# Kernel tuning notes

Measured on AMD Instinct MI355X. Metric: run time of the kernel, lower is better.

Reference implementation:

```python
import jax, jax.numpy as jnp
import numpy as np

L, E, S, V, B, T = 6, 768, 1024, 32000, 2, 1024
FF = 4 * E
EPS = 1e-5

def _layernorm(v, w, b):
    m = jnp.mean(v, axis=-1, keepdims=True)
    var = jnp.mean((v - m) ** 2, axis=-1, keepdims=True)
    return (v - m) * jax.lax.rsqrt(var + EPS) * w + b

def setup_inputs() -> dict:
    key = jax.random.key(0)
    ks = jax.random.split(key, 12)
    s = 0.02
    n = lambda k, shp: (jax.random.normal(k, shp, jnp.float32) * s)
    return {
        "x": jax.random.randint(ks[0], (B, T), 0, V),
        "tok_emb": n(ks[1], (V, E)),
        "pos_emb": jax.random.normal(ks[2], (S, E), jnp.float32),  # nn.Parameter(randn)
        "Wq": n(ks[3], (L, E, E)), "bq": jnp.zeros((L, E), jnp.float32),
        "Wk": n(ks[4], (L, E, E)), "bk": jnp.zeros((L, E), jnp.float32),
        "Wv": n(ks[5], (L, E, E)), "bv": jnp.zeros((L, E), jnp.float32),
        "ln1w": jnp.ones((L, E), jnp.float32), "ln1b": jnp.zeros((L, E), jnp.float32),
        "W1": n(ks[6], (L, E, FF)), "b1": jnp.zeros((L, FF), jnp.float32),
        "W2": n(ks[7], (L, FF, E)), "b2": jnp.zeros((L, E), jnp.float32),
        "ln2w": jnp.ones((L, E), jnp.float32), "ln2b": jnp.zeros((L, E), jnp.float32),
        "Wo": n(ks[8], (E, V)), "bo": jnp.zeros((V,), jnp.float32),
    }

def reference(x, tok_emb, pos_emb, Wq, bq, Wk, bk, Wv, bv, ln1w, ln1b,
              W1, b1, W2, b2, ln2w, ln2b, Wo, bo):
    t = x.shape[1]
    h = tok_emb[x] + pos_emb[:t]  # [B,T,E]
    scale = jnp.sqrt(jnp.float32(E))
    tril = jnp.tril(jnp.ones((t, t), bool))

    def layer(h, p):
        wq, bq_, wk, bk_, wv, bv_, l1w, l1b, w1, b1_, w2, b2_, l2w, l2b = p
        Q = h @ wq + bq_
        K = h @ wk + bk_
        Vv = h @ wv + bv_
        scores = jnp.einsum('btd,bsd->bts', Q, K) / scale
        # original adds a mask of 1.0 on allowed positions, -inf elsewhere
        masked = jnp.where(tril, scores + 1.0, -jnp.inf)
        A = jax.nn.softmax(masked, axis=-1)
        att = jnp.einsum('bts,bsd->btd', A, Vv)
        h1 = _layernorm(h + att, l1w, l1b)
        ffn = jax.nn.relu(h1 @ w1 + b1_) @ w2 + b2_
        h2 = _layernorm(ffn + h1, l2w, l2b)
        return h2, None

    params = (Wq, bq, Wk, bk, Wv, bv, ln1w, ln1b, W1, b1, W2, b2, ln2w, ln2b)
    h, _ = jax.lax.scan(layer, h, params)
    return h @ Wo + bo  # [B,T,V]
```

## Files before the change

### kernel.cpp

```cpp
#include <hip/hip_runtime.h>
#include <stdint.h>

typedef __bf16 v8bf __attribute__((ext_vector_type(8)));
typedef float  v4f  __attribute__((ext_vector_type(4)));
typedef float  v2f  __attribute__((ext_vector_type(2)));

__device__ __forceinline__ float bf2f(uint16_t h) {
    union { uint32_t u; float f; } x; x.u = ((uint32_t)h) << 16; return x.f;
}
__device__ __forceinline__ uint16_t f2bf(float f) {
    union { float f; uint32_t u; } x; x.f = f;
    uint32_t r = x.u + 0x7fffu + ((x.u >> 16) & 1u);
    return (uint16_t)(r >> 16);
}

__device__ __forceinline__ void gload16(const uint16_t* g, uint16_t* l) {
    __builtin_amdgcn_global_load_lds((const __attribute__((address_space(1))) void*)g,
                                     (__attribute__((address_space(3))) void*)l, 16, 0, 0);
}

__global__ void k_embed(const int* __restrict__ x, const float* __restrict__ tok,
                        const float* __restrict__ pos, float* __restrict__ hf,
                        uint16_t* __restrict__ hb)
{
    int i = blockIdx.x;
    int t = i & 1023;
    int tk = x[i];
    const float* te = tok + (long)tk * 768;
    const float* pe = pos + (long)t * 768;
    for (int j = threadIdx.x; j < 768; j += 256) {
        float v = te[j] + pe[j];
        hf[(long)i * 768 + j] = v;
        hb[(long)i * 768 + j] = f2bf(v);
    }
}

template<typename SrcT>
__global__ void k_transpose(const SrcT* __restrict__ src, uint16_t* __restrict__ dst,
                            int ldS, int ldD, long sBatch, long dBatch)
{
    __shared__ float tile[32][33];
    src += (long)blockIdx.z * sBatch;
    dst += (long)blockIdx.z * dBatch;
    int c0 = blockIdx.x * 32, r0 = blockIdx.y * 32;
    int tx = threadIdx.x, ty = threadIdx.y;
    #pragma unroll
    for (int i = 0; i < 4; ++i) {
        int r = r0 + ty + i * 8;
        SrcT s = src[(long)r * ldS + c0 + tx];
        float v;
        if constexpr (sizeof(SrcT) == 4) v = (float)s; else v = bf2f((uint16_t)s);
        tile[ty + i * 8][tx] = v;
    }
    __syncthreads();
    #pragma unroll
    for (int i = 0; i < 4; ++i) {
        int c = c0 + ty + i * 8;
        dst[(long)c * ldD + r0 + tx] = f2bf(tile[tx][ty + i * 8]);
    }
}

__global__ void k_concat3(const float* __restrict__ a, const float* __restrict__ b,
                          const float* __restrict__ c, float* __restrict__ out)
{
    int l = blockIdx.y;
    const float* s = (blockIdx.x == 0) ? a : ((blockIdx.x == 1) ? b : c);
    s += (long)l * 768;
    for (int j = threadIdx.x; j < 768; j += 256)
        out[(long)l * 2304 + blockIdx.x * 768 + j] = s[j];
}

template<typename OutT, bool BIAS, bool RELU, bool RES>
__global__ __launch_bounds__(256, 3)
void k_gemmp(const uint16_t* __restrict__ A, const uint16_t* __restrict__ BT,
             OutT* __restrict__ C, const float* __restrict__ bias,
             const float* __restrict__ res,
             int K, int lda, int ldb, int ldc,
             long bsA, long bsB, long bsC, float scale, int causal)
{
    const int nwg = gridDim.x * gridDim.y;
    int lin = blockIdx.y * gridDim.x + blockIdx.x;
    {
        int q = nwg >> 3, r = nwg & 7, x = lin & 7, i = lin >> 3;
        lin = (x < r ? x * (q + 1) : r * (q + 1) + (x - r) * q) + i;
    }
    const int mt = lin % gridDim.y;
    const int nt = lin / gridDim.y;

    if (causal == 1 && nt * 64 >= (mt + 1) * 128) return;
    const int Keff = (causal == 2) ? ((mt + 1) * 128 < K ? (mt + 1) * 128 : K) : K;
    const int KT = Keff >> 6;

    __shared__ uint16_t lds[2][192 * 64];
    const int tid  = threadIdx.x;
    const int lane = tid & 63;
    const int bz   = blockIdx.z;
    const uint16_t* Ab = A + (long)bz * bsA + (long)mt * 128 * lda;
    const uint16_t* Bb = BT + (long)bz * bsB + (long)nt * 64 * ldb;

    const int wm = (tid >> 6) >> 1, wn = (tid >> 6) & 1;
    const int fr = lane & 15, fq = lane >> 4;

    const int srow = tid >> 3;
    const int sl   = tid & 7;

    v4f acc[4][2];
    #pragma unroll
    for (int m = 0; m < 4; ++m)
        #pragma unroll
        for (int n = 0; n < 2; ++n) acc[m][n] = (v4f){0.f, 0.f, 0.f, 0.f};

    auto stage = [&](int t, int buf) {
        const int ko = t * 64;
        #pragma unroll
        for (int p = 0; p < 6; ++p) {
            int row = p * 32 + srow;
            int ss  = (sl ^ (row & 7)) * 8;
            const uint16_t* g = (p < 4) ? (Ab + (long)row * lda + ko + ss)
                                        : (Bb + (long)(row - 128) * ldb + ko + ss);
            gload16(g, &lds[buf][p * 2048 + tid * 8]);
        }
    };

    stage(0, 0);

    for (int kti = 0; kti < KT; ++kti) {
        asm volatile("s_waitcnt vmcnt(0)" ::: "memory");
        __builtin_amdgcn_s_barrier();
        if (kti + 1 < KT) stage(kti + 1, (kti + 1) & 1);

        const uint16_t* l = &lds[kti & 1][0];
        #pragma unroll
        for (int kk = 0; kk < 2; ++kk) {
            const int sIdx = kk * 4 + fq;
            v8bf ag[4], bg[2];
            #pragma unroll
            for (int m = 0; m < 4; ++m) {
                int r = wm * 64 + m * 16 + fr;
                ag[m] = *(const v8bf*)&l[r * 64 + ((sIdx ^ (r & 7)) << 3)];
            }
            #pragma unroll
            for (int n = 0; n < 2; ++n) {
                int r = 128 + wn * 32 + n * 16 + fr;
                bg[n] = *(const v8bf*)&l[r * 64 + ((sIdx ^ (r & 7)) << 3)];
            }
            __builtin_amdgcn_s_setprio(1);
            #pragma unroll
            for (int m = 0; m < 4; ++m)
                #pragma unroll
                for (int n = 0; n < 2; ++n)
                    acc[m][n] = __builtin_amdgcn_mfma_f32_16x16x32_bf16(ag[m], bg[n], acc[m][n], 0, 0, 0);
            __builtin_amdgcn_s_setprio(0);
        }
    }

    OutT* Cb = C + (long)bz * bsC + (long)mt * 128 * ldc + nt * 64;
    const float* Rb = RES ? (res + (long)bz * bsC + (long)mt * 128 * ldc + nt * 64) : nullptr;
    #pragma unroll
    for (int n = 0; n < 2; ++n) {
        int col = wn * 32 + n * 16 + fr;
        float bv = BIAS ? bias[nt * 64 + col] : 0.f;
        #pragma unroll
        for (int m = 0; m < 4; ++m) {
            #pragma unroll
            for (int r = 0; r < 4; ++r) {
                int row = wm * 64 + m * 16 + fq * 4 + r;
                float v = acc[m][n][r] * scale + bv;
                if (RES) v += Rb[(long)row * ldc + col];
                if (RELU) v = fmaxf(v, 0.f);
                if constexpr (sizeof(OutT) == 4) Cb[(long)row * ldc + col] = v;
                else                             Cb[(long)row * ldc + col] = f2bf(v);
            }
        }
    }
}

__global__ __launch_bounds__(512, 4)
void k_glogits(const uint16_t* __restrict__ A, const uint16_t* __restrict__ BT,
               float* __restrict__ C, const float* __restrict__ bias,
               int K, int lda, int ldb, int ldc, float scale)
{
    __shared__ uint16_t lds[576 * 64];

    const int nwg = gridDim.x * gridDim.y;
    int lin = blockIdx.y * gridDim.x + blockIdx.x;
    {
        int q = nwg >> 3, r = nwg & 7, x = lin & 7, i = lin >> 3;
        lin = (x < r ? x * (q + 1) : r * (q + 1) + (x - r) * q) + i;
    }
    const int nt = lin % gridDim.x;
    const int mt = lin / gridDim.x;

    const int tid  = threadIdx.x;
    const int lane = tid & 63;
    const int wid  = tid >> 6;
    const int wm = wid >> 1, wn = wid & 1;
    const int fr = lane & 15, fq = lane >> 4;

    const uint16_t* Ab = A  + (long)mt * 512 * lda;
    const uint16_t* Bb = BT + (long)nt * 64 * ldb;

    const int srow = tid >> 3;
    const int sl   = tid & 7;
    const int KT   = K >> 6;

    v4f acc[8][2];
    #pragma unroll
    for (int m = 0; m < 8; ++m)
        #pragma unroll
        for (int n = 0; n < 2; ++n) acc[m][n] = (v4f){0.f, 0.f, 0.f, 0.f};

    for (int kti = 0; kti < KT; ++kti) {
        const int ko = kti * 64;
        #pragma unroll
        for (int p = 0; p < 9; ++p) {
            int row = p * 64 + srow;
            int ss  = (sl ^ (row & 7)) * 8;
            const uint16_t* g = (p < 8) ? (Ab + (long)row * lda + ko + ss)
                                        : (Bb + (long)(row - 512) * ldb + ko + ss);
            gload16(g, &lds[p * 4096 + tid * 8]);
        }
        asm volatile("s_waitcnt vmcnt(0)" ::: "memory");
        __builtin_amdgcn_s_barrier();

        #pragma unroll
        for (int kk = 0; kk < 2; ++kk) {
            const int sIdx = kk * 4 + fq;
            v8bf ag[8], bg[2];
            #pragma unroll
            for (int m = 0; m < 8; ++m) {
                int r = wm * 128 + m * 16 + fr;
                ag[m] = *(const v8bf*)&lds[r * 64 + ((sIdx ^ (r & 7)) << 3)];
            }
            #pragma unroll
            for (int n = 0; n < 2; ++n) {
                int r = 512 + wn * 32 + n * 16 + fr;
                bg[n] = *(const v8bf*)&lds[r * 64 + ((sIdx ^ (r & 7)) << 3)];
            }
            __builtin_amdgcn_s_setprio(1);
            #pragma unroll
            for (int m = 0; m < 8; ++m)
                #pragma unroll
                for (int n = 0; n < 2; ++n)
                    acc[m][n] = __builtin_amdgcn_mfma_f32_16x16x32_bf16(ag[m], bg[n], acc[m][n], 0, 0, 0);
            __builtin_amdgcn_s_setprio(0);
        }
        __builtin_amdgcn_s_barrier();
    }

    float* lf = (float*)lds;
    float bcol = bias[nt * 64 + lane];
    const long Cb0 = (long)(mt * 512) * ldc + nt * 64;

    #pragma unroll
    for (int c = 0; c < 8; ++c) {
        __syncthreads();
        if (wm == (c >> 1)) {
            const int mo = (c & 1) * 4;
            #pragma unroll
            for (int m = 0; m < 4; ++m)
                #pragma unroll
                for (int n = 0; n < 2; ++n)
                    #pragma unroll
                    for (int r = 0; r < 4; ++r)
                        lf[(m * 16 + fq * 4 + r) * 65 + wn * 32 + n * 16 + fr] = acc[mo + m][n][r];
        }
        __syncthreads();
        #pragma unroll
        for (int rr = 0; rr < 8; ++rr) {
            int row = wid * 8 + rr;
            float v = lf[row * 65 + lane];
            __builtin_nontemporal_store(v * scale + bcol,
                &C[Cb0 + (long)(c * 64 + row) * ldc + lane]);
        }
    }
}

__global__ void k_softmax(const float* __restrict__ S, uint16_t* __restrict__ P)
{
    int t = blockIdx.x, b = blockIdx.y;
    const float* row = S + ((long)b * 1024 + t) * 1024;
    uint16_t* pr = P + ((long)b * 1024 + t) * 1024;
    int limit = (t & ~127) + 128;
    int s0 = threadIdx.x * 4;
    float vals[4] = {0.f, 0.f, 0.f, 0.f};
    if (s0 < limit) {
        float4 vv = *(const float4*)(row + s0);
        vals[0] = vv.x; vals[1] = vv.y; vals[2] = vv.z; vals[3] = vv.w;
    }
    float mx = -1e30f;
    #pragma unroll
    for (int j = 0; j < 4; ++j) if (s0 + j <= t) mx = fmaxf(mx, vals[j]);
    #pragma unroll
    for (int o = 32; o; o >>= 1) mx = fmaxf(mx, __shfl_xor(mx, o));
    __shared__ float red[8];
    int wave = threadIdx.x >> 6, lane = threadIdx.x & 63;
    if (lane == 0) red[wave] = mx;
    __syncthreads();
    mx = fmaxf(fmaxf(red[0], red[1]), fmaxf(red[2], red[3]));
    float e[4]; float sum = 0.f;
    #pragma unroll
    for (int j = 0; j < 4; ++j) { e[j] = (s0 + j <= t) ? __expf(vals[j] - mx) : 0.f; sum += e[j]; }
    #pragma unroll
    for (int o = 32; o; o >>= 1) sum += __shfl_xor(sum, o);
    if (lane == 0) red[4 + wave] = sum;
    __syncthreads();
    sum = red[4] + red[5] + red[6] + red[7];
    float inv = 1.f / sum;
    if (s0 < limit) {
        #pragma unroll
        for (int j = 0; j < 4; ++j) pr[s0 + j] = f2bf(e[j] * inv);
    }
}

__global__ void k_ln(const float* __restrict__ a,
                     const float* __restrict__ w, const float* __restrict__ bias,
                     float* __restrict__ outf, uint16_t* __restrict__ outb)
{
    int row = blockIdx.x;
    const float* ar = a + (long)row * 768;
    float v[3]; float s1 = 0.f, s2 = 0.f;
    #pragma unroll
    for (int i = 0; i < 3; ++i) {
        int e = threadIdx.x + i * 256;
        v[i] = ar[e];
        s1 += v[i]; s2 += v[i] * v[i];
    }
    #pragma unroll
    for (int o = 32; o; o >>= 1) { s1 += __shfl_xor(s1, o); s2 += __shfl_xor(s2, o); }
    __shared__ float red[8];
    int wave = threadIdx.x >> 6, lane = threadIdx.x & 63;
    if (lane == 0) { red[wave] = s1; red[4 + wave] = s2; }
    __syncthreads();
    s1 = red[0] + red[1] + red[2] + red[3];
    s2 = red[4] + red[5] + red[6] + red[7];
    float mean = s1 * (1.f / 768.f);
    float var  = s2 * (1.f / 768.f) - mean * mean;
    float rstd = rsqrtf(var + 1e-5f);
    #pragma unroll
    for (int i = 0; i < 3; ++i) {
        int e = threadIdx.x + i * 256;
        float o = (v[i] - mean) * rstd * w[e] + bias[e];
        outf[(long)row * 768 + e] = o;
        outb[(long)row * 768 + e] = f2bf(o);
    }
}

__global__ void k_ln_ffn2(const float* __restrict__ p, long pstride,
                          const float* __restrict__ b2, const float* __restrict__ h1,
                          const float* __restrict__ w, const float* __restrict__ bias,
                          float* __restrict__ outf, uint16_t* __restrict__ outb)
{
    int row = blockIdx.x;
    long base = (long)row * 768;
    float v[3]; float s1 = 0.f, s2 = 0.f;
    #pragma unroll
    for (int i = 0; i < 3; ++i) {
        int e = threadIdx.x + i * 256;
        float acc = b2[e] + h1[base + e];
        #pragma unroll
        for (int s = 0; s < 4; ++s) acc += p[base + e + s * pstride];
        v[i] = acc;
        s1 += acc; s2 += acc * acc;
    }
    #pragma unroll
    for (int o = 32; o; o >>= 1) { s1 += __shfl_xor(s1, o); s2 += __shfl_xor(s2, o); }
    __shared__ float red[8];
    int wave = threadIdx.x >> 6, lane = threadIdx.x & 63;
    if (lane == 0) { red[wave] = s1; red[4 + wave] = s2; }
    __syncthreads();
    s1 = red[0] + red[1] + red[2] + red[3];
    s2 = red[4] + red[5] + red[6] + red[7];
    float mean = s1 * (1.f / 768.f);
    float var  = s2 * (1.f / 768.f) - mean * mean;
    float rstd = rsqrtf(var + 1e-5f);
    #pragma unroll
    for (int i = 0; i < 3; ++i) {
        int e = threadIdx.x + i * 256;
        float o = (v[i] - mean) * rstd * w[e] + bias[e];
        outf[base + e] = o;
        outb[base + e] = f2bf(o);
    }
}

extern "C" void kernel_launch(void* const* d_in, const int* in_sizes, int n_in,
                              void* d_out, int out_size, void* d_ws, size_t ws_size,
                              hipStream_t stream)
{
    const int*   x       = (const int*)d_in[0];
    const float* tok_emb = (const float*)d_in[1];
    const float* pos_emb = (const float*)d_in[2];
    const float* Wq  = (const float*)d_in[3];
    const float* bq  = (const float*)d_in[4];
    const float* Wk  = (const float*)d_in[5];
    const float* bk  = (const float*)d_in[6];
    const float* Wv  = (const float*)d_in[7];
    const float* bv  = (const float*)d_in[8];
    const float* ln1w = (const float*)d_in[9];
    const float* ln1b = (const float*)d_in[10];
    const float* W1  = (const float*)d_in[11];
    const float* b1  = (const float*)d_in[12];
    const float* W2  = (const float*)d_in[13];
    const float* b2  = (const float*)d_in[14];
    const float* ln2w = (const float*)d_in[15];
    const float* ln2b = (const float*)d_in[16];
    const float* Wo  = (const float*)d_in[17];
    const float* bo  = (const float*)d_in[18];
    float* out = (float*)d_out;
    (void)in_sizes; (void)n_in; (void)out_size;

    char* ws = (char*)d_ws;
    size_t off = 0;
    auto alloc = [&](size_t bytes) -> char* {
        char* p = ws + off;
        off = (off + bytes + 255) & ~(size_t)255;
        return p;
    };
    uint16_t* WoT   = (uint16_t*)alloc(32000L * 768 * 2);
    float*    hf    = (float*)alloc(2048L * 768 * 4);
    uint16_t* hb    = (uint16_t*)alloc(2048L * 768 * 2);
    uint16_t* qkv   = (uint16_t*)alloc(2048L * 2304 * 2);
    uint16_t* vT    = (uint16_t*)alloc(2L * 768 * 1024 * 2);
    float*    sc    = (float*)alloc(2L * 1024 * 1024 * 4);
    uint16_t* pr    = (uint16_t*)alloc(2L * 1024 * 1024 * 2);
    float*    hsum  = (float*)alloc(2048L * 768 * 4);
    float*    h1f   = (float*)alloc(2048L * 768 * 4);
    uint16_t* h1b   = (uint16_t*)alloc(2048L * 768 * 2);
    uint16_t* f1    = (uint16_t*)alloc(2048L * 3072 * 2);
    float*    f2p   = (float*)alloc(4L * 2048 * 768 * 4);
    float*    bqkvA = (float*)alloc(6L * 2304 * 4);
    const long PSTR = 2048L * 768;

    size_t mark = off;
    uint16_t* WqkvTA = (uint16_t*)alloc(6L * 2304 * 768 * 2);
    uint16_t* W1TA   = (uint16_t*)alloc(6L * 3072 * 768 * 2);
    uint16_t* W2TA   = (uint16_t*)alloc(6L * 768 * 3072 * 2);
    bool hoist = (off <= ws_size);
    uint16_t *WqkvT = nullptr, *W1T = nullptr, *W2T = nullptr;
    if (!hoist) {
        off = mark;
        WqkvT = (uint16_t*)alloc(2304L * 768 * 2);
        W1T   = (uint16_t*)alloc(3072L * 768 * 2);
        W2T   = (uint16_t*)alloc(768L * 3072 * 2);
    }

    dim3 tb(32, 8);
    const float iscale = 0.036084391824351615f;
    const long EE = 768L * 768;

    k_transpose<float><<<dim3(1000, 24, 1), tb, 0, stream>>>(Wo, WoT, 32000, 768, 0, 0);
    k_embed<<<2048, 256, 0, stream>>>(x, tok_emb, pos_emb, hf, hb);
    k_concat3<<<dim3(3, 6), 256, 0, stream>>>(bq, bk, bv, bqkvA);

    if (hoist) {
        k_transpose<float><<<dim3(24, 24, 6), tb, 0, stream>>>(Wq, WqkvTA,             768, 768, EE, 2304L*768);
        k_transpose<float><<<dim3(24, 24, 6), tb, 0, stream>>>(Wk, WqkvTA + 768L*768,  768, 768, EE, 2304L*768);
        k_transpose<float><<<dim3(24, 24, 6), tb, 0, stream>>>(Wv, WqkvTA + 1536L*768, 768, 768, EE, 2304L*768);
        k_transpose<float><<<dim3(96, 24, 6), tb, 0, stream>>>(W1, W1TA, 3072, 768, 768L*3072, 3072L*768);
        k_transpose<float><<<dim3(24, 96, 6), tb, 0, stream>>>(W2, W2TA, 768, 3072, 3072L*768, 768L*3072);
    }

    for (int l = 0; l < 6; ++l) {
        uint16_t* WqkvL = hoist ? (WqkvTA + l * 2304L * 768) : WqkvT;
        uint16_t* W1L   = hoist ? (W1TA   + l * 3072L * 768) : W1T;
        uint16_t* W2L   = hoist ? (W2TA   + l * 768L * 3072) : W2T;
        if (!hoist) {
            k_transpose<float><<<dim3(24, 24, 1), tb, 0, stream>>>(Wq + l * EE, WqkvT,             768, 768, 0, 0);
            k_transpose<float><<<dim3(24, 24, 1), tb, 0, stream>>>(Wk + l * EE, WqkvT + 768L*768,  768, 768, 0, 0);
            k_transpose<float><<<dim3(24, 24, 1), tb, 0, stream>>>(Wv + l * EE, WqkvT + 1536L*768, 768, 768, 0, 0);
            k_transpose<float><<<dim3(96, 24, 1), tb, 0, stream>>>(W1 + l * 768L * 3072, W1T, 3072, 768, 0, 0);
            k_transpose<float><<<dim3(24, 96, 1), tb, 0, stream>>>(W2 + l * 3072L * 768, W2T, 768, 3072, 0, 0);
        }

        k_gemmp<uint16_t, true, false, false><<<dim3(36, 16, 1), 256, 0, stream>>>(
            hb, WqkvL, qkv, bqkvA + l * 2304, nullptr, 768, 768, 768, 2304, 0, 0, 0, 1.f, 0);
        k_gemmp<float, false, false, false><<<dim3(16, 8, 2), 256, 0, stream>>>(
            qkv, qkv + 768, sc, nullptr, nullptr, 768, 2304, 2304, 1024,
            1024L * 2304, 1024L * 2304, 1024L * 1024, iscale, 1);
        k_softmax<<<dim3(1024, 2), 256, 0, stream>>>(sc, pr);
        k_transpose<uint16_t><<<dim3(24, 32, 2), tb, 0, stream>>>(
            qkv + 1536, vT, 2304, 1024, 1024L * 2304, 768L * 1024);
        k_gemmp<float, false, false, true><<<dim3(12, 8, 2), 256, 0, stream>>>(
            pr, vT, hsum, nullptr, hf, 1024, 1024, 1024, 768,
            1024L * 1024, 768L * 1024, 1024L * 768, 1.f, 2);
        k_ln<<<2048, 256, 0, stream>>>(hsum, ln1w + l * 768, ln1b + l * 768, h1f, h1b);
        k_gemmp<uint16_t, true, true, false><<<dim3(48, 16, 1), 256, 0, stream>>>(
            h1b, W1L, f1, b1 + l * 3072, nullptr, 768, 768, 768, 3072, 0, 0, 0, 1.f, 0);
        k_gemmp<float, false, false, false><<<dim3(12, 16, 4), 256, 0, stream>>>(
            f1, W2L, f2p, nullptr, nullptr, 768, 3072, 3072, 768,
            768, 768, PSTR, 1.f, 0);
        k_ln_ffn2<<<2048, 256, 0, stream>>>(f2p, PSTR, b2 + l * 768, h1f,
                                            ln2w + l * 768, ln2b + l * 768, hf, hb);
    }

    k_glogits<<<dim3(500, 4, 1), 512, 0, stream>>>(
        hb, WoT, out, bo, 768, 768, 768, 32000, 1.f);
}
```

Measured before the change: 815.3 us.

## Retile logits GEMM to 256x256 with double-buffered pipelined LDS staging

Restructures the final vocabulary-projection GEMM from 512x64 tiles to 256x256 tiles, with eight waves laid out 2x4. Global-to-LDS loads now go into a double buffer in half-tile chunks, interleaved with MFMA quarter-blocks, so memory traffic overlaps compute. The epilogue is vectorized to float4 stores. The square tile improves operand reuse and the pipeline hides load latency, at the cost of more LDS (128KB) and higher register pressure, which lowers occupancy to 2 blocks per CU.

```diff
diff --git a/kernel.cpp b/kernel.cpp
--- a/kernel.cpp
+++ b/kernel.cpp
@@ -3,7 +3,6 @@
 
 typedef __bf16 v8bf __attribute__((ext_vector_type(8)));
 typedef float  v4f  __attribute__((ext_vector_type(4)));
-typedef float  v2f  __attribute__((ext_vector_type(2)));
 
 __device__ __forceinline__ float bf2f(uint16_t h) {
     union { uint32_t u; float f; } x; x.u = ((uint32_t)h) << 16; return x.f;
@@ -175,12 +174,51 @@
     }
 }
 
-__global__ __launch_bounds__(512, 4)
+#define STAGE_H(buf, op, half, s)                                                   \
+    do { if ((s) < KS) {                                                            \
+        const uint16_t* Gp_ = (op) ? Bb : Ab;                                       \
+        const int ldg_ = (op) ? ldb : lda;                                          \
+        uint16_t* dst_ = &lds[buf][(op) * 16384 + (half) * 8192];                   \
+        { int rg_ = (half) * 128 + (tid >> 3);                                      \
+          int ss_ = ((tid & 7) ^ (rg_ & 7)) << 3;                                   \
+          gload16(Gp_ + (long)rg_ * ldg_ + (s) * 64 + ss_, dst_ + tid * 8); }       \
+        { int rg_ = (half) * 128 + (tid >> 3) + 64;                                 \
+          int ss_ = ((tid & 7) ^ (rg_ & 7)) << 3;                                   \
+          gload16(Gp_ + (long)rg_ * ldg_ + (s) * 64 + ss_, dst_ + (tid + 512) * 8); } \
+    } } while (0)
+
+#define READ_AG(buf, mh)                                                            \
+    do { _Pragma("unroll") for (int m_ = 0; m_ < 4; ++m_) {                         \
+        int r_ = wm * 128 + (mh) * 64 + m_ * 16 + fr;                               \
+        ag[m_][0] = *(const v8bf*)&lds[buf][r_ * 64 + ((fq ^ (r_ & 7)) << 3)];      \
+        ag[m_][1] = *(const v8bf*)&lds[buf][r_ * 64 + (((4 | fq) ^ (r_ & 7)) << 3)];\
+    } } while (0)
+
+#define READ_BG(buf, nh, BG)                                                        \
+    do { _Pragma("unroll") for (int n_ = 0; n_ < 2; ++n_) {                         \
+        int r_ = wn * 64 + (nh) * 32 + n_ * 16 + fr;                                \
+        BG[n_][0] = *(const v8bf*)&lds[buf][16384 + r_ * 64 + ((fq ^ (r_ & 7)) << 3)]; \
+        BG[n_][1] = *(const v8bf*)&lds[buf][16384 + r_ * 64 + (((4 | fq) ^ (r_ & 7)) << 3)]; \
+    } } while (0)
+
+#define MMAQ(mh, nh, BG)                                                            \
+    do { __builtin_amdgcn_s_setprio(1);                                             \
+        _Pragma("unroll") for (int m_ = 0; m_ < 4; ++m_)                            \
+        _Pragma("unroll") for (int n_ = 0; n_ < 2; ++n_) {                          \
+            acc[(mh)*4+m_][(nh)*2+n_] = __builtin_amdgcn_mfma_f32_16x16x32_bf16(    \
+                ag[m_][0], BG[n_][0], acc[(mh)*4+m_][(nh)*2+n_], 0, 0, 0);          \
+            acc[(mh)*4+m_][(nh)*2+n_] = __builtin_amdgcn_mfma_f32_16x16x32_bf16(    \
+                ag[m_][1], BG[n_][1], acc[(mh)*4+m_][(nh)*2+n_], 0, 0, 0);          \
+        }                                                                           \
+        __builtin_amdgcn_s_setprio(0);                                              \
+    } while (0)
+
+__global__ __launch_bounds__(512, 2)
 void k_glogits(const uint16_t* __restrict__ A, const uint16_t* __restrict__ BT,
                float* __restrict__ C, const float* __restrict__ bias,
                int K, int lda, int ldb, int ldc, float scale)
 {
-    __shared__ uint16_t lds[576 * 64];
+    __shared__ uint16_t lds[2][32768];
 
     const int nwg = gridDim.x * gridDim.y;
     int lin = blockIdx.y * gridDim.x + blockIdx.x;
@@ -194,84 +232,97 @@
     const int tid  = threadIdx.x;
     const int lane = tid & 63;
     const int wid  = tid >> 6;
-    const int wm = wid >> 1, wn = wid & 1;
+    const int wm = wid >> 2, wn = wid & 3;
     const int fr = lane & 15, fq = lane >> 4;
 
-    const uint16_t* Ab = A  + (long)mt * 512 * lda;
-    const uint16_t* Bb = BT + (long)nt * 64 * ldb;
-
-    const int srow = tid >> 3;
-    const int sl   = tid & 7;
-    const int KT   = K >> 6;
-
-    v4f acc[8][2];
+    const uint16_t* Ab = A  + (long)mt * 256 * lda;
+    const uint16_t* Bb = BT + (long)nt * 256 * ldb;
+
+    const int KS  = K >> 6;
+    const int NIT = KS >> 1;
+
+    v4f acc[8][4];
     #pragma unroll
     for (int m = 0; m < 8; ++m)
         #pragma unroll
-        for (int n = 0; n < 2; ++n) acc[m][n] = (v4f){0.f, 0.f, 0.f, 0.f};
-
-    for (int kti = 0; kti < KT; ++kti) {
-        const int ko = kti * 64;
-        #pragma unroll
-        for (int p = 0; p < 9; ++p) {
-            int row = p * 64 + srow;
-            int ss  = (sl ^ (row & 7)) * 8;
-            const uint16_t* g = (p < 8) ? (Ab + (long)row * lda + ko + ss)
-                                        : (Bb + (long)(row - 512) * ldb + ko + ss);
-            gload16(g, &lds[p * 4096 + tid * 8]);
-        }
-        asm volatile("s_waitcnt vmcnt(0)" ::: "memory");
-        __builtin_amdgcn_s_barrier();
-
-        #pragma unroll
-        for (int kk = 0; kk < 2; ++kk) {
-            const int sIdx = kk * 4 + fq;
-            v8bf ag[8], bg[2];
-            #pragma unroll
-            for (int m = 0; m < 8; ++m) {
-                int r = wm * 128 + m * 16 + fr;
-                ag[m] = *(const v8bf*)&lds[r * 64 + ((sIdx ^ (r & 7)) << 3)];
-            }
-            #pragma unroll
-            for (int n = 0; n < 2; ++n) {
-                int r = 512 + wn * 32 + n * 16 + fr;
-                bg[n] = *(const v8bf*)&lds[r * 64 + ((sIdx ^ (r & 7)) << 3)];
-            }
-            __builtin_amdgcn_s_setprio(1);
-            #pragma unroll
-            for (int m = 0; m < 8; ++m)
-                #pragma unroll
-                for (int n = 0; n < 2; ++n)
-                    acc[m][n] = __builtin_amdgcn_mfma_f32_16x16x32_bf16(ag[m], bg[n], acc[m][n], 0, 0, 0);
-            __builtin_amdgcn_s_setprio(0);
-        }
-        __builtin_amdgcn_s_barrier();
+        for (int n = 0; n < 4; ++n) acc[m][n] = (v4f){0.f, 0.f, 0.f, 0.f};
+
+    v8bf ag[4][2], bg0[2][2], bg1[2][2];
+
+    STAGE_H(0, 0, 0, 0);
+    STAGE_H(0, 0, 1, 0);
+    STAGE_H(0, 1, 0, 0);
+    STAGE_H(0, 1, 1, 0);
+    STAGE_H(1, 0, 0, 1);
+
+    for (int i = 0; i < NIT; ++i) {
+        const int s1 = 2 * i + 1;
+        asm volatile("s_waitcnt vmcnt(2)" ::: "memory");
+        __builtin_amdgcn_s_barrier();
+        READ_AG(0, 0); READ_BG(0, 0, bg0);
+        STAGE_H(1, 0, 1, s1);
+        MMAQ(0, 0, bg0);
+        __builtin_amdgcn_s_barrier();
+        READ_BG(0, 1, bg1);
+        STAGE_H(1, 1, 0, s1);
+        MMAQ(0, 1, bg1);
+        __builtin_amdgcn_s_barrier();
+        READ_AG(0, 1);
+        STAGE_H(1, 1, 1, s1);
+        MMAQ(1, 0, bg0);
+        __builtin_amdgcn_s_barrier();
+        STAGE_H(0, 0, 0, s1 + 1);
+        MMAQ(1, 1, bg1);
+        if (i + 1 < NIT) asm volatile("s_waitcnt vmcnt(2)" ::: "memory");
+        else             asm volatile("s_waitcnt vmcnt(0)" ::: "memory");
+        __builtin_amdgcn_s_barrier();
+        READ_AG(1, 0); READ_BG(1, 0, bg0);
+        STAGE_H(0, 0, 1, s1 + 1);
+        MMAQ(0, 0, bg0);
+        __builtin_amdgcn_s_barrier();
+        READ_BG(1, 1, bg1);
+        STAGE_H(0, 1, 0, s1 + 1);
+        MMAQ(0, 1, bg1);
+        __builtin_amdgcn_s_barrier();
+        READ_AG(1, 1);
+        STAGE_H(0, 1, 1, s1 + 1);
+        MMAQ(1, 0, bg0);
+        __builtin_amdgcn_s_barrier();
+        STAGE_H(1, 0, 0, s1 + 2);
+        MMAQ(1, 1, bg1);
     }
 
     float* lf = (float*)lds;
-    float bcol = bias[nt * 64 + lane];
-    const long Cb0 = (long)(mt * 512) * ldc + nt * 64;
-
-    #pragma unroll
-    for (int c = 0; c < 8; ++c) {
+    v4f b4 = *(const v4f*)&bias[nt * 256 + lane * 4];
+    const long Cb0 = (long)(mt * 256) * ldc + nt * 256;
+
+    #pragma unroll
+    for (int c = 0; c < 4; ++c) {
         __syncthreads();
         if (wm == (c >> 1)) {
-            const int mo = (c & 1) * 4;
             #pragma unroll
             for (int m = 0; m < 4; ++m)
                 #pragma unroll
-                for (int n = 0; n < 2; ++n)
+                for (int nh = 0; nh < 2; ++nh)
                     #pragma unroll
-                    for (int r = 0; r < 4; ++r)
-                        lf[(m * 16 + fq * 4 + r) * 65 + wn * 32 + n * 16 + fr] = acc[mo + m][n][r];
+                    for (int n = 0; n < 2; ++n)
+                        #pragma unroll
+                        for (int r = 0; r < 4; ++r)
+                            lf[(m * 16 + fq * 4 + r) * 260 + wn * 64 + nh * 32 + n * 16 + fr]
+                                = acc[(c & 1) * 4 + m][nh * 2 + n][r];
         }
         __syncthreads();
         #pragma unroll
         for (int rr = 0; rr < 8; ++rr) {
             int row = wid * 8 + rr;
-            float v = lf[row * 65 + lane];
-            __builtin_nontemporal_store(v * scale + bcol,
-                &C[Cb0 + (long)(c * 64 + row) * ldc + lane]);
+            v4f v = *(const v4f*)&lf[row * 260 + lane * 4];
+            v4f o;
+            o.x = v.x * scale + b4.x;
+            o.y = v.y * scale + b4.y;
+            o.z = v.z * scale + b4.z;
+            o.w = v.w * scale + b4.w;
+            __builtin_nontemporal_store(o,
+                (v4f*)&C[Cb0 + (long)(c * 64 + row) * ldc + lane * 4]);
         }
     }
 }
@@ -493,6 +544,6 @@
                                             ln2w + l * 768, ln2b + l * 768, hf, hb);
     }
 
-    k_glogits<<<dim3(500, 4, 1), 512, 0, stream>>>(
+    k_glogits<<<dim3(125, 8, 1), 512, 0, stream>>>(
         hb, WoT, out, bo, 768, 768, 768, 32000, 1.f);
 }
```

After: 792.4 us. 2.8% less time.
